# Kernel optimization log

Hardware: AMD Instinct MI355X
Metric: run time of the kernel (lower is better)

## Reference

```python
import jax, jax.numpy as jnp
import numpy as np

N, IN_DIM, HEADS, OUT_DIM = 4096, 256, 4, 64

def setup_inputs() -> dict:
    key = jax.random.key(0)
    k1, k2, k3 = jax.random.split(key, 3)
    h = jax.random.normal(k1, (N, IN_DIM), dtype=jnp.float32)
    W = jax.random.normal(k2, (IN_DIM, HEADS * OUT_DIM), dtype=jnp.float32) * (1.0 / np.sqrt(IN_DIM))
    a = jax.random.normal(k3, (HEADS, 2 * OUT_DIM), dtype=jnp.float32) * 0.1
    return {"h": h, "W": W, "a": a}

def reference(h, W, a):
    # Wh: [N, heads, out_dim]
    Wh = (h @ W).reshape(N, HEADS, OUT_DIM)
    # Split additive attention vector a = [a_dst | a_src]; e[i,j,k] = lrelu(f_i[i,k] + f_j[j,k])
    # This is algebraically identical to LeakyReLU(((Wh_i||Wh_j) * a).sum(-1))
    f_i = jnp.einsum('nhd,hd->nh', Wh, a[:, :OUT_DIM])   # [N, heads]
    f_j = jnp.einsum('nhd,hd->nh', Wh, a[:, OUT_DIM:])   # [N, heads]
    e = jax.nn.leaky_relu(f_i[:, None, :] + f_j[None, :, :], negative_slope=0.2)  # [N,N,heads]
    attn = jax.nn.softmax(e, axis=1)  # softmax over source nodes j
    # dropout is identity in eval mode
    out = jnp.einsum('ijk,jkl->ikl', attn, Wh)  # [N, heads, out_dim]
    out = out.reshape(N, HEADS * OUT_DIM)       # concat=True
    return out, attn
```

## Files before the change

### kernel.cpp

```cpp
#include <hip/hip_runtime.h>
#include <math.h>

#define NN 4096
#define IN_DIM 256
#define HEADS 4
#define OUT_DIM 64

__device__ __forceinline__ float fexp(float x){ return __expf(x); }

__global__ void k_gw(const float* __restrict__ h, const float* __restrict__ W,
                     const float* __restrict__ a,
                     float* __restrict__ Wh, float* __restrict__ fi, float* __restrict__ fjT,
                     float* __restrict__ E1j, float* __restrict__ E2j){
    __shared__ float4 hs4[8][64];
    const int i0 = blockIdx.x * 8;
    const int t  = threadIdx.x;
    const int hh = t >> 6, d = t & 63;
    {
        const float4* h4 = (const float4*)h;
        hs4[t >> 6][t & 63]         = h4[(i0 + (t >> 6)) * 64 + (t & 63)];
        hs4[(t >> 6) + 4][t & 63]   = h4[(i0 + (t >> 6) + 4) * 64 + (t & 63)];
    }
    __syncthreads();
    float acc[8];
    #pragma unroll
    for (int r = 0; r < 8; ++r) acc[r] = 0.f;
    #pragma unroll 4
    for (int kq = 0; kq < 64; ++kq) {
        const int k = kq * 4;
        const float w0 = W[(k + 0) * 256 + t];
        const float w1 = W[(k + 1) * 256 + t];
        const float w2 = W[(k + 2) * 256 + t];
        const float w3 = W[(k + 3) * 256 + t];
        #pragma unroll
        for (int r = 0; r < 8; ++r) {
            const float4 hv = hs4[r][kq];
            acc[r] = fmaf(hv.x, w0, acc[r]);
            acc[r] = fmaf(hv.y, w1, acc[r]);
            acc[r] = fmaf(hv.z, w2, acc[r]);
            acc[r] = fmaf(hv.w, w3, acc[r]);
        }
    }
    const float aD = a[hh * 128 + d];
    const float aS = a[hh * 128 + 64 + d];
    #pragma unroll
    for (int r = 0; r < 8; ++r) {
        Wh[(i0 + r) * 256 + t] = acc[r];
        float p1 = acc[r] * aD, p2 = acc[r] * aS;
        #pragma unroll
        for (int off = 32; off; off >>= 1) {
            p1 += __shfl_down(p1, off);
            p2 += __shfl_down(p2, off);
        }
        if (d == 0) {
            const int n = i0 + r;
            fi[n * 4 + hh]   = p1;
            fjT[hh * NN + n] = p2;
            E1j[n * 4 + hh]  = fexp(p2);
            E2j[n * 4 + hh]  = fexp(0.2f * p2);
        }
    }
}

__global__ void k_rp(const float* __restrict__ fjT, const float* __restrict__ Wh,
                     float* __restrict__ fs, float* __restrict__ Whp){
    const int j0 = blockIdx.x * 8;
    const int t = threadIdx.x;
    const int hh = t >> 6, d = t & 63;
    const int base = hh * NN;
    float v[8]; int cnt[8];
    #pragma unroll
    for (int r = 0; r < 8; ++r) { v[r] = fjT[base + j0 + r]; cnt[r] = 0; }
    #pragma unroll 4
    for (int m = 0; m < 64; ++m) {
        const int jp = d + m * 64;
        const float x = fjT[base + jp];
        #pragma unroll
        for (int r = 0; r < 8; ++r)
            cnt[r] += (x < v[r] || (x == v[r] && jp < (j0 + r))) ? 1 : 0;
    }
    #pragma unroll
    for (int r = 0; r < 8; ++r) {
        int c = cnt[r];
        #pragma unroll
        for (int off = 32; off; off >>= 1) c += __shfl_down(c, off);
        const int rank = __shfl(c, 0);
        if (d == 0) fs[base + rank] = v[r];
        Whp[(size_t)(base + rank) * 64 + d] = Wh[(j0 + r) * 256 + hh * 64 + d];
    }
}

__global__ void k_chunks(const float* __restrict__ fs, const float* __restrict__ Whp,
                         float* __restrict__ r1, float* __restrict__ r2x,
                         float* __restrict__ rz1, float* __restrict__ rz2x,
                         float* __restrict__ cs1, float* __restrict__ cs2,
                         float* __restrict__ cz1, float* __restrict__ cz2){
    const int b = blockIdx.x;
    const int H = b >> 6, c = b & 63;
    const int t = threadIdx.x;
    const int w = t >> 6, d = t & 63;
    const int base = H * NN;
    const int qw = c * 64 + w * 16;
    float wv[16], e1s[16], e2s[16];
    #pragma unroll
    for (int s = 0; s < 16; ++s) {
        const int q = qw + s;
        const float f = fs[base + q];
        e1s[s] = fexp(f);
        e2s[s] = fexp(0.2f * f);
        wv[s]  = Whp[(size_t)(base + q) * 64 + d];
    }
    float p2[16], s1[16], lz1[16], lz2[16];
    float acc2 = 0.f, z2 = 0.f;
    #pragma unroll
    for (int s = 0; s < 16; ++s) {
        p2[s] = acc2; lz2[s] = z2;
        acc2 += e2s[s] * wv[s]; z2 += e2s[s];
    }
    float acc1 = 0.f, z1 = 0.f;
    #pragma unroll
    for (int s = 15; s >= 0; --s) {
        acc1 += e1s[s] * wv[s]; z1 += e1s[s];
        s1[s] = acc1; lz1[s] = z1;
    }
    __shared__ float t1[4][64], t2[4][64], tz1[4], tz2[4];
    t1[w][d] = acc1; t2[w][d] = acc2;
    if (d == 0) { tz1[w] = z1; tz2[w] = z2; }
    __syncthreads();
    float off1 = 0.f, off2 = 0.f, zo1 = 0.f, zo2 = 0.f;
    #pragma unroll
    for (int w2 = 0; w2 < 4; ++w2) {
        if (w2 > w) { off1 += t1[w2][d]; zo1 += tz1[w2]; }
        if (w2 < w) { off2 += t2[w2][d]; zo2 += tz2[w2]; }
    }
    #pragma unroll
    for (int s = 0; s < 16; ++s) {
        const int q = qw + s;
        r1 [(size_t)(base + q) * 64 + d] = off1 + s1[s];
        r2x[(size_t)(base + q) * 64 + d] = off2 + p2[s];
        if (d == 0) {
            rz1 [base + q] = zo1 + lz1[s];
            rz2x[base + q] = zo2 + lz2[s];
        }
    }
    if (w == 0) {
        cs1[b * 64 + d] = off1 + acc1;
        if (d == 0) cz1[b] = zo1 + z1;
    }
    if (w == 3) {
        cs2[b * 64 + d] = off2 + acc2;
        if (d == 0) cz2[b] = zo2 + z2;
    }
}

__global__ void k_scan(const float* __restrict__ cs1, const float* __restrict__ cs2,
                       const float* __restrict__ cz1, const float* __restrict__ cz2,
                       float* __restrict__ S1, float* __restrict__ S2,
                       float* __restrict__ Z1, float* __restrict__ Z2){
    const int H = blockIdx.x;
    const int t = threadIdx.x;
    if (t < 64) {
        const int d = t; float acc = 0.f;
        S1[(H * 65 + 64) * 64 + d] = 0.f;
        #pragma unroll 8
        for (int c = 63; c >= 0; --c) { acc += cs1[(H * 64 + c) * 64 + d]; S1[(H * 65 + c) * 64 + d] = acc; }
    } else if (t < 128) {
        const int d = t - 64; float acc = 0.f;
        S2[(H * 65 + 0) * 64 + d] = 0.f;
        #pragma unroll 8
        for (int c = 0; c < 64; ++c) { acc += cs2[(H * 64 + c) * 64 + d]; S2[(H * 65 + c + 1) * 64 + d] = acc; }
    } else if (t == 128) {
        float acc = 0.f; Z1[H * 65 + 64] = 0.f;
        for (int c = 63; c >= 0; --c) { acc += cz1[H * 64 + c]; Z1[H * 65 + c] = acc; }
    } else if (t == 129) {
        float acc = 0.f; Z2[H * 65 + 0] = 0.f;
        for (int c = 0; c < 64; ++c) { acc += cz2[H * 64 + c]; Z2[H * 65 + c + 1] = acc; }
    }
}

__global__ void k_q(const float* __restrict__ fi, const float* __restrict__ fs,
                    const float* __restrict__ r1, const float* __restrict__ r2x,
                    const float* __restrict__ rz1, const float* __restrict__ rz2x,
                    const float* __restrict__ S1, const float* __restrict__ S2,
                    const float* __restrict__ Z1, const float* __restrict__ Z2,
                    float* __restrict__ out, float* __restrict__ thrE,
                    float* __restrict__ A1, float* __restrict__ A2){
    const int i = blockIdx.x;
    const int t = threadIdx.x;
    const int hh = t >> 6, d = t & 63;
    const int base = hh * NN;
    const float s = fi[i * 4 + hh];
    const float thr = -s;
    const unsigned long long m1 = __ballot(fs[base + d * 64] < thr);
    const int k1 = __popcll(m1);
    int p = 0;
    if (k1 > 0) {
        const int cc = k1 - 1;
        const unsigned long long m2 = __ballot(fs[base + cc * 64 + d] < thr);
        p = cc * 64 + __popcll(m2);
    }
    float a1, a2, z1, z2;
    if (p == NN) {
        a1 = 0.f; z1 = 0.f;
        a2 = S2[(hh * 65 + 64) * 64 + d]; z2 = Z2[hh * 65 + 64];
    } else {
        const int c = p >> 6;
        a1 = r1 [(size_t)(base + p) * 64 + d] + S1[(hh * 65 + c + 1) * 64 + d];
        z1 = rz1[base + p]                    + Z1[hh * 65 + c + 1];
        a2 = r2x[(size_t)(base + p) * 64 + d] + S2[(hh * 65 + c) * 64 + d];
        z2 = rz2x[base + p]                   + Z2[hh * 65 + c];
    }
    const float E1 = fexp(s), E2 = fexp(0.2f * s);
    const float iz = 1.f / (E1 * z1 + E2 * z2);
    out[i * 256 + t] = (E1 * a1 + E2 * a2) * iz;
    if (d == 0) {
        thrE[i * 4 + hh] = fexp(thr);
        A1[i * 4 + hh]   = E1 * iz;
        A2[i * 4 + hh]   = E2 * iz;
    }
}

__global__ void k_attn(const float4* __restrict__ E1j4, const float4* __restrict__ E2j4,
                       const float4* __restrict__ thrE4, const float4* __restrict__ A14,
                       const float4* __restrict__ A24, float4* __restrict__ attn){
    const int i = blockIdx.x;
    const float4 th = thrE4[i];
    const float4 a1 = A14[i];
    const float4 a2 = A24[i];
    float4* __restrict__ row = attn + (size_t)i * NN;
    const int t = threadIdx.x;
    #pragma unroll
    for (int it = 0; it < 16; ++it) {
        const int j = it * 256 + t;
        const float4 e1 = E1j4[j];
        const float4 e2 = E2j4[j];
        float4 o;
        o.x = (e1.x >= th.x) ? a1.x * e1.x : a2.x * e2.x;
        o.y = (e1.y >= th.y) ? a1.y * e1.y : a2.y * e2.y;
        o.z = (e1.z >= th.z) ? a1.z * e1.z : a2.z * e2.z;
        o.w = (e1.w >= th.w) ? a1.w * e1.w : a2.w * e2.w;
        row[j] = o;
    }
}

extern "C" void kernel_launch(void* const* d_in, const int* in_sizes, int n_in,
                              void* d_out, int out_size, void* d_ws, size_t ws_size,
                              hipStream_t stream) {
    const float* h = (const float*)d_in[0];
    const float* W = (const float*)d_in[1];
    const float* a = (const float*)d_in[2];
    float* out = (float*)d_out;
    float* ws  = (float*)d_ws;

    float* Wh   = ws;
    float* Whp  = Wh   + 1048576;
    float* fi   = Whp  + 1048576;
    float* fjT  = fi   + 16384;
    float* E1j  = fjT  + 16384;
    float* E2j  = E1j  + 16384;
    float* fs   = E2j  + 16384;
    float* cs1  = fs   + 16384;
    float* cs2  = cs1  + 16384;
    float* cz1  = cs2  + 16384;
    float* cz2  = cz1  + 256;
    float* S1   = cz2  + 256;
    float* S2   = S1   + 16640;
    float* Z1   = S2   + 16640;
    float* Z2   = Z1   + 260;
    float* r1   = Z2   + 260;
    float* r2x  = r1   + 1048576;
    float* rz1  = r2x  + 1048576;
    float* rz2x = rz1  + 16384;
    float* thrE = rz2x + 16384;
    float* A1   = thrE + 16384;
    float* A2   = A1   + 16384;

    k_gw    <<<NN / 8, 256, 0, stream>>>(h, W, a, Wh, fi, fjT, E1j, E2j);
    k_rp    <<<NN / 8, 256, 0, stream>>>(fjT, Wh, fs, Whp);
    k_chunks<<<HEADS * 64, 256, 0, stream>>>(fs, Whp, r1, r2x, rz1, rz2x, cs1, cs2, cz1, cz2);
    k_scan  <<<HEADS, 256, 0, stream>>>(cs1, cs2, cz1, cz2, S1, S2, Z1, Z2);
    k_q     <<<NN, 256, 0, stream>>>(fi, fs, r1, r2x, rz1, rz2x, S1, S2, Z1, Z2, out, thrE, A1, A2);

    float* attn = out + (NN * HEADS * OUT_DIM);
    k_attn  <<<NN, 256, 0, stream>>>((const float4*)E1j, (const float4*)E2j,
                                     (const float4*)thrE, (const float4*)A1,
                                     (const float4*)A2, (float4*)attn);
}
```

Baseline: 132.0 us.

## Drop materialized in-chunk prefix sums; recompute partial chunk sums in query kernel

The chunk kernel no longer writes full per-position prefix arrays r1/r2x/rz1/rz2x (about 8 MB of writes and reads). It now computes only per-chunk totals, and the query kernel recomputes the partial sum within the boundary chunk by looping over 64 entries. The attention-write kernel is split into four blocks per row and uses nontemporal stores, as does the output write. This trades heavy global memory traffic for 64 extra loop iterations with exp per query thread.

```diff
diff --git a/kernel.cpp b/kernel.cpp
--- a/kernel.cpp
+++ b/kernel.cpp
@@ -5,6 +5,8 @@
 #define IN_DIM 256
 #define HEADS 4
 #define OUT_DIM 64
+
+typedef float f32x4 __attribute__((ext_vector_type(4)));
 
 __device__ __forceinline__ float fexp(float x){ return __expf(x); }
 
@@ -91,66 +93,25 @@
 }
 
 __global__ void k_chunks(const float* __restrict__ fs, const float* __restrict__ Whp,
-                         float* __restrict__ r1, float* __restrict__ r2x,
-                         float* __restrict__ rz1, float* __restrict__ rz2x,
                          float* __restrict__ cs1, float* __restrict__ cs2,
                          float* __restrict__ cz1, float* __restrict__ cz2){
-    const int b = blockIdx.x;
-    const int H = b >> 6, c = b & 63;
-    const int t = threadIdx.x;
-    const int w = t >> 6, d = t & 63;
-    const int base = H * NN;
-    const int qw = c * 64 + w * 16;
-    float wv[16], e1s[16], e2s[16];
-    #pragma unroll
-    for (int s = 0; s < 16; ++s) {
-        const int q = qw + s;
-        const float f = fs[base + q];
-        e1s[s] = fexp(f);
-        e2s[s] = fexp(0.2f * f);
-        wv[s]  = Whp[(size_t)(base + q) * 64 + d];
-    }
-    float p2[16], s1[16], lz1[16], lz2[16];
-    float acc2 = 0.f, z2 = 0.f;
-    #pragma unroll
-    for (int s = 0; s < 16; ++s) {
-        p2[s] = acc2; lz2[s] = z2;
-        acc2 += e2s[s] * wv[s]; z2 += e2s[s];
-    }
-    float acc1 = 0.f, z1 = 0.f;
-    #pragma unroll
-    for (int s = 15; s >= 0; --s) {
-        acc1 += e1s[s] * wv[s]; z1 += e1s[s];
-        s1[s] = acc1; lz1[s] = z1;
-    }
-    __shared__ float t1[4][64], t2[4][64], tz1[4], tz2[4];
-    t1[w][d] = acc1; t2[w][d] = acc2;
-    if (d == 0) { tz1[w] = z1; tz2[w] = z2; }
-    __syncthreads();
-    float off1 = 0.f, off2 = 0.f, zo1 = 0.f, zo2 = 0.f;
-    #pragma unroll
-    for (int w2 = 0; w2 < 4; ++w2) {
-        if (w2 > w) { off1 += t1[w2][d]; zo1 += tz1[w2]; }
-        if (w2 < w) { off2 += t2[w2][d]; zo2 += tz2[w2]; }
-    }
-    #pragma unroll
-    for (int s = 0; s < 16; ++s) {
-        const int q = qw + s;
-        r1 [(size_t)(base + q) * 64 + d] = off1 + s1[s];
-        r2x[(size_t)(base + q) * 64 + d] = off2 + p2[s];
-        if (d == 0) {
-            rz1 [base + q] = zo1 + lz1[s];
-            rz2x[base + q] = zo2 + lz2[s];
-        }
-    }
-    if (w == 0) {
-        cs1[b * 64 + d] = off1 + acc1;
-        if (d == 0) cz1[b] = zo1 + z1;
-    }
-    if (w == 3) {
-        cs2[b * 64 + d] = off2 + acc2;
-        if (d == 0) cz2[b] = zo2 + z2;
-    }
+    const int c = blockIdx.x;
+    const int t = threadIdx.x;
+    const int hh = t >> 6, d = t & 63;
+    const int base = hh * NN;
+    const int q0 = c * 64;
+    float a1 = 0.f, a2 = 0.f, z1 = 0.f, z2 = 0.f;
+    #pragma unroll 4
+    for (int q = q0; q < q0 + 64; ++q) {
+        const float f  = fs[base + q];
+        const float e1 = fexp(f), e2 = fexp(0.2f * f);
+        const float wv = Whp[(size_t)(base + q) * 64 + d];
+        a1 += e1 * wv; z1 += e1;
+        a2 += e2 * wv; z2 += e2;
+    }
+    cs1[(hh * 64 + c) * 64 + d] = a1;
+    cs2[(hh * 64 + c) * 64 + d] = a2;
+    if (d == 0) { cz1[hh * 64 + c] = z1; cz2[hh * 64 + c] = z2; }
 }
 
 __global__ void k_scan(const float* __restrict__ cs1, const float* __restrict__ cs2,
@@ -179,8 +140,7 @@
 }
 
 __global__ void k_q(const float* __restrict__ fi, const float* __restrict__ fs,
-                    const float* __restrict__ r1, const float* __restrict__ r2x,
-                    const float* __restrict__ rz1, const float* __restrict__ rz2x,
+                    const float* __restrict__ Whp,
                     const float* __restrict__ S1, const float* __restrict__ S2,
                     const float* __restrict__ Z1, const float* __restrict__ Z2,
                     float* __restrict__ out, float* __restrict__ thrE,
@@ -199,20 +159,23 @@
         const unsigned long long m2 = __ballot(fs[base + cc * 64 + d] < thr);
         p = cc * 64 + __popcll(m2);
     }
-    float a1, a2, z1, z2;
-    if (p == NN) {
-        a1 = 0.f; z1 = 0.f;
-        a2 = S2[(hh * 65 + 64) * 64 + d]; z2 = Z2[hh * 65 + 64];
-    } else {
-        const int c = p >> 6;
-        a1 = r1 [(size_t)(base + p) * 64 + d] + S1[(hh * 65 + c + 1) * 64 + d];
-        z1 = rz1[base + p]                    + Z1[hh * 65 + c + 1];
-        a2 = r2x[(size_t)(base + p) * 64 + d] + S2[(hh * 65 + c) * 64 + d];
-        z2 = rz2x[base + p]                   + Z2[hh * 65 + c];
-    }
+    const int c = min(p >> 6, 63);
+    float a1 = 0.f, a2 = 0.f, z1 = 0.f, z2 = 0.f;
+    const int q0 = c * 64;
+    #pragma unroll 4
+    for (int q = q0; q < q0 + 64; ++q) {
+        const float f  = fs[base + q];
+        const float wv = Whp[(size_t)(base + q) * 64 + d];
+        if (q >= p) { const float e = fexp(f);        a1 += e * wv; z1 += e; }
+        else        { const float e = fexp(0.2f * f); a2 += e * wv; z2 += e; }
+    }
+    a1 += S1[(hh * 65 + c + 1) * 64 + d];
+    z1 += Z1[hh * 65 + c + 1];
+    a2 += S2[(hh * 65 + c) * 64 + d];
+    z2 += Z2[hh * 65 + c];
     const float E1 = fexp(s), E2 = fexp(0.2f * s);
     const float iz = 1.f / (E1 * z1 + E2 * z2);
-    out[i * 256 + t] = (E1 * a1 + E2 * a2) * iz;
+    __builtin_nontemporal_store((E1 * a1 + E2 * a2) * iz, &out[i * 256 + t]);
     if (d == 0) {
         thrE[i * 4 + hh] = fexp(thr);
         A1[i * 4 + hh]   = E1 * iz;
@@ -220,26 +183,29 @@
     }
 }
 
-__global__ void k_attn(const float4* __restrict__ E1j4, const float4* __restrict__ E2j4,
-                       const float4* __restrict__ thrE4, const float4* __restrict__ A14,
-                       const float4* __restrict__ A24, float4* __restrict__ attn){
-    const int i = blockIdx.x;
-    const float4 th = thrE4[i];
-    const float4 a1 = A14[i];
-    const float4 a2 = A24[i];
-    float4* __restrict__ row = attn + (size_t)i * NN;
-    const int t = threadIdx.x;
-    #pragma unroll
-    for (int it = 0; it < 16; ++it) {
+__global__ void k_attn(const f32x4* __restrict__ E1j4, const f32x4* __restrict__ E2j4,
+                       const f32x4* __restrict__ thrE4, const f32x4* __restrict__ A14,
+                       const f32x4* __restrict__ A24, f32x4* __restrict__ attn){
+    const int bid = blockIdx.x;
+    const int i = bid >> 2, qtr = bid & 3;
+    const int t = threadIdx.x;
+    const f32x4 th = thrE4[i];
+    const f32x4 c1 = A14[i];
+    const f32x4 c2 = A24[i];
+    const f32x4* __restrict__ e1p = E1j4 + qtr * 1024;
+    const f32x4* __restrict__ e2p = E2j4 + qtr * 1024;
+    f32x4* __restrict__ row = attn + (size_t)i * NN + qtr * 1024;
+    #pragma unroll
+    for (int it = 0; it < 4; ++it) {
         const int j = it * 256 + t;
-        const float4 e1 = E1j4[j];
-        const float4 e2 = E2j4[j];
-        float4 o;
-        o.x = (e1.x >= th.x) ? a1.x * e1.x : a2.x * e2.x;
-        o.y = (e1.y >= th.y) ? a1.y * e1.y : a2.y * e2.y;
-        o.z = (e1.z >= th.z) ? a1.z * e1.z : a2.z * e2.z;
-        o.w = (e1.w >= th.w) ? a1.w * e1.w : a2.w * e2.w;
-        row[j] = o;
+        const f32x4 e1 = e1p[j];
+        const f32x4 e2 = e2p[j];
+        f32x4 o;
+        o.x = (e1.x >= th.x) ? c1.x * e1.x : c2.x * e2.x;
+        o.y = (e1.y >= th.y) ? c1.y * e1.y : c2.y * e2.y;
+        o.z = (e1.z >= th.z) ? c1.z * e1.z : c2.z * e2.z;
+        o.w = (e1.w >= th.w) ? c1.w * e1.w : c2.w * e2.w;
+        __builtin_nontemporal_store(o, &row[j]);
     }
 }
 
@@ -267,22 +233,18 @@
     float* S2   = S1   + 16640;
     float* Z1   = S2   + 16640;
     float* Z2   = Z1   + 260;
-    float* r1   = Z2   + 260;
-    float* r2x  = r1   + 1048576;
-    float* rz1  = r2x  + 1048576;
-    float* rz2x = rz1  + 16384;
-    float* thrE = rz2x + 16384;
+    float* thrE = Z2   + 260;
     float* A1   = thrE + 16384;
     float* A2   = A1   + 16384;
 
     k_gw    <<<NN / 8, 256, 0, stream>>>(h, W, a, Wh, fi, fjT, E1j, E2j);
     k_rp    <<<NN / 8, 256, 0, stream>>>(fjT, Wh, fs, Whp);
-    k_chunks<<<HEADS * 64, 256, 0, stream>>>(fs, Whp, r1, r2x, rz1, rz2x, cs1, cs2, cz1, cz2);
+    k_chunks<<<64, 256, 0, stream>>>(fs, Whp, cs1, cs2, cz1, cz2);
     k_scan  <<<HEADS, 256, 0, stream>>>(cs1, cs2, cz1, cz2, S1, S2, Z1, Z2);
-    k_q     <<<NN, 256, 0, stream>>>(fi, fs, r1, r2x, rz1, rz2x, S1, S2, Z1, Z2, out, thrE, A1, A2);
+    k_q     <<<NN, 256, 0, stream>>>(fi, fs, Whp, S1, S2, Z1, Z2, out, thrE, A1, A2);
 
     float* attn = out + (NN * HEADS * OUT_DIM);
-    k_attn  <<<NN, 256, 0, stream>>>((const float4*)E1j, (const float4*)E2j,
-                                     (const float4*)thrE, (const float4*)A1,
-                                     (const float4*)A2, (float4*)attn);
-}
+    k_attn  <<<NN * 4, 256, 0, stream>>>((const f32x4*)E1j, (const f32x4*)E2j,
+                                         (const f32x4*)thrE, (const f32x4*)A1,
+                                         (const f32x4*)A2, (f32x4*)attn);
+}
```

New measurement: 172.6 us. 1.31x slower.
